# Kernel tuning notes

Measured on AMD Instinct MI355X. Metric: run time of the kernel, lower is better.

## Reference

```python
import jax, jax.numpy as jnp
import numpy as np

N_NODES = 50000
N_EDGES = 800000
IN_FEATS = 512
OUT_FEATS = 512
DROP_P = 0.1


def setup_inputs() -> dict:
    key = jax.random.key(0)
    k1, k2, k3, k4, k5 = jax.random.split(key, 5)
    x = jax.random.normal(k1, (N_NODES, IN_FEATS), dtype=jnp.float32)
    edge_w = jax.random.uniform(k2, (N_EDGES,), dtype=jnp.float32)
    W = jax.random.normal(k3, (IN_FEATS, OUT_FEATS), dtype=jnp.float32) * (1.0 / np.sqrt(IN_FEATS))
    b = jnp.zeros((OUT_FEATS,), dtype=jnp.float32)
    edge_src = jax.random.randint(k4, (N_EDGES,), 0, N_NODES, dtype=jnp.int32)
    edge_dst = jnp.sort(jax.random.randint(k5, (N_EDGES,), 0, N_NODES, dtype=jnp.int32))
    return {"x": x, "edge_w": edge_w, "W": W, "b": b,
            "edge_src": edge_src, "edge_dst": edge_dst}


def reference(x, edge_w, W, b, edge_src, edge_dst):
    # Dropout (train mode, p=0.1) with a fixed key for determinism.
    keep = jax.random.bernoulli(jax.random.key(42), 1.0 - DROP_P, x.shape)
    xd = jnp.where(keep, x / (1.0 - DROP_P), 0.0)
    # Sparse adjacency matmul: out[dst] += adj_w * x[src]  (torch.spmm(adj, x))
    msgs = xd[edge_src] * edge_w[:, None]          # [E, in_feats]
    agg = jax.ops.segment_sum(msgs, edge_dst, num_segments=N_NODES)  # [N, in_feats]
    # Linear + ReLU activation
    return jax.nn.relu(agg @ W + b)
```

## Files before the change

### kernel.cpp

```cpp
#include <hip/hip_runtime.h>
#include <hip/hip_bf16.h>
#include <stdint.h>


#define N_NODESC 50000
#define N_EDGESC 800000
#define FEATS    512
#define TOT_ELEMS (N_NODESC * FEATS)

#define DROP_BLKS   12500
#define WCONV_BLKS  1024
#define ROWP_BLKS   3126
#define PREP_BLKS   (DROP_BLKS + WCONV_BLKS + ROWP_BLKS)

typedef unsigned int u32;
typedef unsigned short u16;
typedef __attribute__((ext_vector_type(8))) short short8;
typedef __attribute__((ext_vector_type(4))) float floatx4;

__device__ __forceinline__ void tf_round(u32& a, u32& b, int r) {
  a += b;
  b = (b << r) | (b >> (32 - r));
  b ^= a;
}

__device__ __forceinline__ void threefry(u32& x0, u32& x1) {
  const u32 k0 = 0u, k1 = 42u, k2 = 0x1BD11BDAu ^ 0u ^ 42u;
  x0 += k0; x1 += k1;
  tf_round(x0,x1,13); tf_round(x0,x1,15); tf_round(x0,x1,26); tf_round(x0,x1,6);
  x0 += k1; x1 += k2 + 1u;
  tf_round(x0,x1,17); tf_round(x0,x1,29); tf_round(x0,x1,16); tf_round(x0,x1,24);
  x0 += k2; x1 += k0 + 2u;
  tf_round(x0,x1,13); tf_round(x0,x1,15); tf_round(x0,x1,26); tf_round(x0,x1,6);
  x0 += k0; x1 += k1 + 3u;
  tf_round(x0,x1,17); tf_round(x0,x1,29); tf_round(x0,x1,16); tf_round(x0,x1,24);
  x0 += k1; x1 += k2 + 4u;
  tf_round(x0,x1,13); tf_round(x0,x1,15); tf_round(x0,x1,26); tf_round(x0,x1,6);
  x0 += k2; x1 += k0 + 5u;
}

__device__ __forceinline__ u16 f2bf(float f) {
  u32 u = __float_as_uint(f);
  u32 r = (u + 0x7FFFu + ((u >> 16) & 1u)) >> 16;
  return (u16)r;
}

__global__ __launch_bounds__(256) void prep_kernel(const float* __restrict__ x,
                                                   u16* __restrict__ xd,
                                                   const float* __restrict__ W,
                                                   u16* __restrict__ WbT,
                                                   const int* __restrict__ dst,
                                                   int* __restrict__ rowptr) {
  int b = blockIdx.x;
  if (b < DROP_BLKS) {
    int t = b * 256 + threadIdx.x;
    int j0 = t * 8;
    float4 xa = *(const float4*)(x + j0);
    float4 xb = *(const float4*)(x + j0 + 4);
    float xs[8] = {xa.x, xa.y, xa.z, xa.w, xb.x, xb.y, xb.z, xb.w};
    u16 r[8];
#pragma unroll
    for (int q = 0; q < 8; ++q) {
      u32 a = 0u, c = (u32)(j0 + q);
      threefry(a, c);
      u32 bits = a ^ c;
      float u = __uint_as_float((bits >> 9) | 0x3F800000u) - 1.0f;
      float m = (u < 0.9f) ? (1.0f / 0.9f) : 0.0f;
      r[q] = f2bf(xs[q] * m);
    }
    uint4 o;
    o.x = (u32)r[0] | ((u32)r[1] << 16);
    o.y = (u32)r[2] | ((u32)r[3] << 16);
    o.z = (u32)r[4] | ((u32)r[5] << 16);
    o.w = (u32)r[6] | ((u32)r[7] << 16);
    *(uint4*)(xd + j0) = o;
  } else if (b < DROP_BLKS + WCONV_BLKS) {
    int t = (b - DROP_BLKS) * 256 + threadIdx.x;
    int k = t >> 9, n = t & 511;
    WbT[n * 512 + k] = f2bf(W[t]);
  } else {
    int e = (b - DROP_BLKS - WCONV_BLKS) * 256 + threadIdx.x;
    if (e > N_EDGESC) return;
    int d  = (e < N_EDGESC) ? dst[e] : N_NODESC;
    int pd = (e > 0) ? dst[e - 1] : -1;
    for (int n = pd + 1; n <= d; ++n) rowptr[n] = e;
  }
}

__device__ __forceinline__ void agg_fma(float* acc, float w, const uint4& v) {
  u32 a[4] = {v.x, v.y, v.z, v.w};
#pragma unroll
  for (int p = 0; p < 4; ++p) {
    acc[2*p]   += w * __uint_as_float(a[p] << 16);
    acc[2*p+1] += w * __uint_as_float(a[p] & 0xFFFF0000u);
  }
}

__global__ __launch_bounds__(256) void agg_kernel(const u16* __restrict__ xd,
                                                  const float* __restrict__ ew,
                                                  const int* __restrict__ src,
                                                  const int* __restrict__ rowptr,
                                                  u16* __restrict__ agg) {
  int node = blockIdx.x * 4 + (threadIdx.x >> 6);
  if (node >= N_NODESC) return;
  int lane = threadIdx.x & 63;
  int lo = rowptr[node];
  int hi = rowptr[node + 1];
  float acc[8] = {0.f,0.f,0.f,0.f,0.f,0.f,0.f,0.f};

  int e = lo;
  for (; e + 8 <= hi; e += 8) {
    uint4 v[8]; float w[8];
#pragma unroll
    for (int q = 0; q < 8; ++q) {
      int s = src[e + q];
      w[q] = ew[e + q];
      v[q] = ((const uint4*)(xd + (size_t)s * FEATS))[lane];
    }
#pragma unroll
    for (int q = 0; q < 8; ++q) agg_fma(acc, w[q], v[q]);
  }
  if (e + 4 <= hi) {
    uint4 v[4]; float w[4];
#pragma unroll
    for (int q = 0; q < 4; ++q) {
      int s = src[e + q];
      w[q] = ew[e + q];
      v[q] = ((const uint4*)(xd + (size_t)s * FEATS))[lane];
    }
#pragma unroll
    for (int q = 0; q < 4; ++q) agg_fma(acc, w[q], v[q]);
    e += 4;
  }
  for (; e < hi; ++e) {
    float w = ew[e];
    int s = src[e];
    uint4 v = ((const uint4*)(xd + (size_t)s * FEATS))[lane];
    agg_fma(acc, w, v);
  }

  uint4 o;
  o.x = (u32)f2bf(acc[0]) | ((u32)f2bf(acc[1]) << 16);
  o.y = (u32)f2bf(acc[2]) | ((u32)f2bf(acc[3]) << 16);
  o.z = (u32)f2bf(acc[4]) | ((u32)f2bf(acc[5]) << 16);
  o.w = (u32)f2bf(acc[6]) | ((u32)f2bf(acc[7]) << 16);
  ((uint4*)(agg + (size_t)node * FEATS))[lane] = o;
}

#define BM 128
#define BN 256
#define BK 32

__global__ __launch_bounds__(512, 4) void gemm_kernel(const u16* __restrict__ A,
                                                      const u16* __restrict__ BT,
                                                      const float* __restrict__ bias,
                                                      float* __restrict__ out) {
  __shared__ __align__(16) u16 Asm[2][BM * BK];
  __shared__ __align__(16) u16 Bsm[2][BN * BK];

  const int tid  = threadIdx.x;
  const int lane = tid & 63;
  const int w    = tid >> 6;
  const int m0 = blockIdx.x * BM;
  const int n0 = blockIdx.y * BN;
  const int wm = (w >> 2) * 64;
  const int wn = (w & 3) * 64;
  const int lm   = lane & 15;
  const int quad = lane >> 4;
  const int srow = lane >> 2;
  const int scol = (lane & 3) * 8;

  int a_gm = m0 + w * 16 + srow;
  if (a_gm > N_NODESC - 1) a_gm = N_NODESC - 1;
  const u16* a_src = A + (size_t)a_gm * 512 + scol;
  const u16* b_src0 = BT + (size_t)(n0 + w * 32 + srow) * 512 + scol;
  const u16* b_src1 = BT + (size_t)(n0 + w * 32 + 16 + srow) * 512 + scol;

#define STAGE(buf, k0)                                                        \
  do {                                                                        \
    __builtin_amdgcn_global_load_lds(                                         \
        (const __attribute__((address_space(1))) void*)(a_src + (k0)),        \
        (__attribute__((address_space(3))) void*)((char*)Asm[buf] + w * 1024 + lane * 16), \
        16, 0, 0);                                                            \
    __builtin_amdgcn_global_load_lds(                                         \
        (const __attribute__((address_space(1))) void*)(b_src0 + (k0)),       \
        (__attribute__((address_space(3))) void*)((char*)Bsm[buf] + (w * 2) * 1024 + lane * 16), \
        16, 0, 0);                                                            \
    __builtin_amdgcn_global_load_lds(                                         \
        (const __attribute__((address_space(1))) void*)(b_src1 + (k0)),       \
        (__attribute__((address_space(3))) void*)((char*)Bsm[buf] + (w * 2 + 1) * 1024 + lane * 16), \
        16, 0, 0);                                                            \
  } while (0)

  floatx4 acc[4][4];
#pragma unroll
  for (int i = 0; i < 4; ++i)
#pragma unroll
    for (int j = 0; j < 4; ++j) acc[i][j] = (floatx4)0.0f;

  STAGE(0, 0);
  __syncthreads();

#pragma unroll 1
  for (int t = 0; t < 512 / BK; ++t) {
    const int cur = t & 1;
    if (t < 512 / BK - 1) STAGE(cur ^ 1, (t + 1) * BK);

    short8 af[4], bfr[4];
#pragma unroll
    for (int i = 0; i < 4; ++i)
      af[i] = *(const short8*)(Asm[cur] + (wm + i * 16 + lm) * BK + quad * 8);
#pragma unroll
    for (int j = 0; j < 4; ++j)
      bfr[j] = *(const short8*)(Bsm[cur] + (wn + j * 16 + lm) * BK + quad * 8);
#pragma unroll
    for (int i = 0; i < 4; ++i)
#pragma unroll
      for (int j = 0; j < 4; ++j)
        acc[i][j] = __builtin_amdgcn_mfma_f32_16x16x32_bf16(af[i], bfr[j], acc[i][j], 0, 0, 0);

    __syncthreads();
  }
#undef STAGE

#pragma unroll
  for (int j = 0; j < 4; ++j) {
    int col = n0 + wn + j * 16 + lm;
    float bv = bias[col];
#pragma unroll
    for (int i = 0; i < 4; ++i) {
      int row0 = m0 + wm + i * 16 + quad * 4;
#pragma unroll
      for (int r = 0; r < 4; ++r) {
        int row = row0 + r;
        if (row < N_NODESC) {
          float v = acc[i][j][r] + bv;
          out[(size_t)row * 512 + col] = v > 0.0f ? v : 0.0f;
        }
      }
    }
  }
}

extern "C" void kernel_launch(void* const* d_in, const int* in_sizes, int n_in,
                              void* d_out, int out_size, void* d_ws, size_t ws_size,
                              hipStream_t stream) {
  const float* x  = (const float*)d_in[0];
  const float* ew = (const float*)d_in[1];
  const float* W  = (const float*)d_in[2];
  const float* b  = (const float*)d_in[3];
  const int* esrc = (const int*)d_in[4];
  const int* edst = (const int*)d_in[5];
  float* out = (float*)d_out;

  char* ws = (char*)d_ws;
  u16* xd    = (u16*)ws;
  u16* agg   = (u16*)(ws + (size_t)TOT_ELEMS * 2);
  u16* WbT   = (u16*)(ws + (size_t)TOT_ELEMS * 4);
  int* rowp  = (int*)(ws + (size_t)TOT_ELEMS * 4 + 512 * 512 * 2);
  (void)ws_size; (void)n_in; (void)in_sizes; (void)out_size;

  hipLaunchKernelGGL(prep_kernel,  dim3(PREP_BLKS), dim3(256), 0, stream,
                     x, xd, W, WbT, edst, rowp);
  hipLaunchKernelGGL(agg_kernel,   dim3((N_NODESC + 3) / 4), dim3(256), 0, stream,
                     xd, ew, esrc, rowp, agg);
  hipLaunchKernelGGL(gemm_kernel,  dim3((N_NODESC + BM - 1) / BM, 512 / BN), dim3(512), 0, stream,
                     agg, WbT, b, out);
}
```

Measured before the change: 359.0 us.

## Swizzle GEMM LDS layout and prefetch two stages ahead with explicit waitcnt

Applies an XOR swizzle to the LDS column placement for the A and B tiles, so the MFMA fragment reads avoid bank conflicts. It also restructures the K loop into a deeper software pipeline: two stages are issued up front, and each iteration uses an explicit s_waitcnt vmcnt(3) plus raw barriers instead of __syncthreads. Loads for stage t+2 are issued after computing stage t. This adds more load/compute overlap and cheaper LDS reads, but relies on manual vmcnt accounting being correct.

```diff
diff --git a/kernel.cpp b/kernel.cpp
--- a/kernel.cpp
+++ b/kernel.cpp
@@ -150,6 +150,7 @@
 #define BM 128
 #define BN 256
 #define BK 32
+#define NT (512 / BK)
 
 __global__ __launch_bounds__(512, 4) void gemm_kernel(const u16* __restrict__ A,
                                                       const u16* __restrict__ BT,
@@ -167,12 +168,14 @@
   const int wn = (w & 3) * 64;
   const int lm   = lane & 15;
   const int quad = lane >> 4;
+  const int sqz = ((quad ^ (lm & 3)) << 4);
+
   const int srow = lane >> 2;
-  const int scol = (lane & 3) * 8;
+  const int scol = (((lane & 3) ^ (srow & 3)) * 8);
 
   int a_gm = m0 + w * 16 + srow;
   if (a_gm > N_NODESC - 1) a_gm = N_NODESC - 1;
-  const u16* a_src = A + (size_t)a_gm * 512 + scol;
+  const u16* a_src  = A  + (size_t)a_gm * 512 + scol;
   const u16* b_src0 = BT + (size_t)(n0 + w * 32 + srow) * 512 + scol;
   const u16* b_src1 = BT + (size_t)(n0 + w * 32 + 16 + srow) * 512 + scol;
 
@@ -180,18 +183,34 @@
   do {                                                                        \
     __builtin_amdgcn_global_load_lds(                                         \
         (const __attribute__((address_space(1))) void*)(a_src + (k0)),        \
-        (__attribute__((address_space(3))) void*)((char*)Asm[buf] + w * 1024 + lane * 16), \
+        (__attribute__((address_space(3))) void*)((char*)Asm[buf] + w * 1024),\
         16, 0, 0);                                                            \
     __builtin_amdgcn_global_load_lds(                                         \
         (const __attribute__((address_space(1))) void*)(b_src0 + (k0)),       \
-        (__attribute__((address_space(3))) void*)((char*)Bsm[buf] + (w * 2) * 1024 + lane * 16), \
+        (__attribute__((address_space(3))) void*)((char*)Bsm[buf] + w * 2048),\
         16, 0, 0);                                                            \
     __builtin_amdgcn_global_load_lds(                                         \
         (const __attribute__((address_space(1))) void*)(b_src1 + (k0)),       \
-        (__attribute__((address_space(3))) void*)((char*)Bsm[buf] + (w * 2 + 1) * 1024 + lane * 16), \
+        (__attribute__((address_space(3))) void*)((char*)Bsm[buf] + w * 2048 + 1024), \
         16, 0, 0);                                                            \
   } while (0)
 
+#define COMPUTE(buf)                                                          \
+  do {                                                                        \
+    short8 af[4], bfr[4];                                                     \
+    _Pragma("unroll")                                                         \
+    for (int i = 0; i < 4; ++i)                                               \
+      af[i] = *(const short8*)((const char*)Asm[buf] + (wm + i * 16 + lm) * 64 + sqz); \
+    _Pragma("unroll")                                                         \
+    for (int j = 0; j < 4; ++j)                                               \
+      bfr[j] = *(const short8*)((const char*)Bsm[buf] + (wn + j * 16 + lm) * 64 + sqz); \
+    _Pragma("unroll")                                                         \
+    for (int i = 0; i < 4; ++i)                                               \
+      _Pragma("unroll")                                                       \
+      for (int j = 0; j < 4; ++j)                                             \
+        acc[i][j] = __builtin_amdgcn_mfma_f32_16x16x32_bf16(af[i], bfr[j], acc[i][j], 0, 0, 0); \
+  } while (0)
+
   floatx4 acc[4][4];
 #pragma unroll
   for (int i = 0; i < 4; ++i)
@@ -199,29 +218,26 @@
     for (int j = 0; j < 4; ++j) acc[i][j] = (floatx4)0.0f;
 
   STAGE(0, 0);
-  __syncthreads();
+  STAGE(1, BK);
 
 #pragma unroll 1
-  for (int t = 0; t < 512 / BK; ++t) {
+  for (int t = 0; t < NT - 2; ++t) {
     const int cur = t & 1;
-    if (t < 512 / BK - 1) STAGE(cur ^ 1, (t + 1) * BK);
-
-    short8 af[4], bfr[4];
-#pragma unroll
-    for (int i = 0; i < 4; ++i)
-      af[i] = *(const short8*)(Asm[cur] + (wm + i * 16 + lm) * BK + quad * 8);
-#pragma unroll
-    for (int j = 0; j < 4; ++j)
-      bfr[j] = *(const short8*)(Bsm[cur] + (wn + j * 16 + lm) * BK + quad * 8);
-#pragma unroll
-    for (int i = 0; i < 4; ++i)
-#pragma unroll
-      for (int j = 0; j < 4; ++j)
-        acc[i][j] = __builtin_amdgcn_mfma_f32_16x16x32_bf16(af[i], bfr[j], acc[i][j], 0, 0, 0);
-
-    __syncthreads();
-  }
+    asm volatile("s_waitcnt vmcnt(3)" ::: "memory");
+    __builtin_amdgcn_s_barrier();
+    COMPUTE(cur);
+    __builtin_amdgcn_s_barrier();
+    STAGE(cur, (t + 2) * BK);
+  }
+  asm volatile("s_waitcnt vmcnt(3)" ::: "memory");
+  __builtin_amdgcn_s_barrier();
+  COMPUTE((NT - 2) & 1);
+  asm volatile("s_waitcnt vmcnt(0)" ::: "memory");
+  __builtin_amdgcn_s_barrier();
+  COMPUTE((NT - 1) & 1);
+
 #undef STAGE
+#undef COMPUTE
 
 #pragma unroll
   for (int j = 0; j < 4; ++j) {
```

New measurement: 361.3 us. No clear change (+0.7%).
